# Kernel tuning notes

Hardware: AMD Instinct MI355X
Metric: run time of the kernel (lower is better)

Reference implementation:

```python
import jax, jax.numpy as jnp
import numpy as np

N_NODES = 100000
N_EDGES = 1600000
HIDDEN = 64
N_MID = 3  # num_layers=5 -> 1 first + 3 middle + 1 last


def setup_inputs() -> dict:
    key = jax.random.key(0)
    ks = jax.random.split(key, 12)
    x = jax.random.normal(ks[0], (N_NODES, 1), dtype=jnp.float32)
    edge_index = jax.random.randint(ks[1], (2, N_EDGES), 0, N_NODES, dtype=jnp.int32)
    edge_weight = jax.random.uniform(ks[2], (N_EDGES,), dtype=jnp.float32)
    s0 = 1.0  # fan_in=1
    sh = 1.0 / np.sqrt(HIDDEN)
    Wrel0 = jax.random.normal(ks[3], (HIDDEN, 1), dtype=jnp.float32) * s0
    brel0 = jax.random.normal(ks[4], (HIDDEN,), dtype=jnp.float32) * s0
    Wroot0 = jax.random.normal(ks[5], (HIDDEN, 1), dtype=jnp.float32) * s0
    Wrel_mid = jax.random.normal(ks[6], (N_MID, HIDDEN, HIDDEN), dtype=jnp.float32) * sh
    brel_mid = jax.random.normal(ks[7], (N_MID, HIDDEN), dtype=jnp.float32) * sh
    Wroot_mid = jax.random.normal(ks[8], (N_MID, HIDDEN, HIDDEN), dtype=jnp.float32) * sh
    WrelL = jax.random.normal(ks[9], (1, HIDDEN), dtype=jnp.float32) * sh
    brelL = jax.random.normal(ks[10], (1,), dtype=jnp.float32) * sh
    WrootL = jax.random.normal(ks[11], (1, HIDDEN), dtype=jnp.float32) * sh
    return {"x": x, "edge_index": edge_index, "edge_weight": edge_weight,
            "Wrel0": Wrel0, "brel0": brel0, "Wroot0": Wroot0,
            "Wrel_mid": Wrel_mid, "brel_mid": brel_mid, "Wroot_mid": Wroot_mid,
            "WrelL": WrelL, "brelL": brelL, "WrootL": WrootL}


def reference(x, edge_index, edge_weight, Wrel0, brel0, Wroot0,
              Wrel_mid, brel_mid, Wroot_mid, WrelL, brelL, WrootL):
    src = edge_index[0]
    dst = edge_index[1]
    n = x.shape[0]

    def conv(h, Wrel, brel, Wroot):
        # PyG GraphConv(aggr='add'): lin_rel(sum_j w_ij * h_j) + lin_root(h_i)
        msg = h[src] * edge_weight[:, None]          # [E, C]
        agg = jax.ops.segment_sum(msg, dst, num_segments=n)  # [N, C]
        return agg @ Wrel.T + brel + h @ Wroot.T

    # dropout omitted (deterministic reference); relu after all but last layer
    h = jax.nn.relu(conv(x, Wrel0, brel0, Wroot0))
    for i in range(Wrel_mid.shape[0]):
        h = jax.nn.relu(conv(h, Wrel_mid[i], brel_mid[i], Wroot_mid[i]))
    return conv(h, WrelL, brelL, WrootL)  # [N, 1]
```

## Files before the change

### kernel.cpp

```cpp
#include <hip/hip_runtime.h>
#include <stdint.h>


#define NN 100000
#define NE 1600000
#define HID 64
#define NBKT 391
#define CAP 8192
#define PMAX (NBKT * CAP)
#define TILE 4096
#define EPT 16
#define NTILE ((NE + TILE - 1) / TILE)

typedef __attribute__((ext_vector_type(8))) short bf16x8;
typedef __attribute__((ext_vector_type(4))) float f32x4;
typedef __attribute__((ext_vector_type(2))) unsigned int u32x2;
typedef __attribute__((ext_vector_type(4))) unsigned int u32x4;

__device__ __forceinline__ uint32_t rne_bf16(float v) {
    uint32_t u = __float_as_uint(v);
    return (u + 0x7fffu + ((u >> 16) & 1u)) >> 16;
}


__global__ __launch_bounds__(256) void k_bpart(const int* __restrict__ src,
                                               const int* __restrict__ dst,
                                               const float* __restrict__ w,
                                               int* __restrict__ bcur,
                                               int2* __restrict__ bpairs) {
    __shared__ int  hcnt[NBKT];
    __shared__ int  hoff[NBKT];
    __shared__ int  hadj[NBKT];
    __shared__ int  sc0[512];
    __shared__ int  sc1[512];
    __shared__ int2 sT[TILE];
    __shared__ int  sAdj[TILE];
    int tile0 = blockIdx.x * TILE;
    int t = threadIdx.x;
    for (int i = t; i < NBKT; i += 256) hcnt[i] = 0;
    __syncthreads();

    int   pk[EPT];
    int   bk[EPT];
    float wv[EPT];
    #pragma unroll
    for (int k = 0; k < EPT; k++) {
        int e = tile0 + t + k * 256;
        if (e < NE) {
            int d = dst[e];
            int b = d >> 8;
            pk[k] = (src[e] << 8) | (d & 255);
            wv[k] = w[e];
            bk[k] = b;
            atomicAdd(&hcnt[b], 1);
        } else {
            bk[k] = -1;
        }
    }
    __syncthreads();

    sc0[t]       = (t < NBKT) ? hcnt[t] : 0;
    sc0[t + 256] = (t + 256 < NBKT) ? hcnt[t + 256] : 0;
    __syncthreads();
    int* cur = sc0;
    int* oth = sc1;
    for (int off = 1; off < 512; off <<= 1) {
        int v0 = cur[t]       + ((t       >= off) ? cur[t - off]       : 0);
        int v1 = cur[t + 256] + ((t + 256 >= off) ? cur[t + 256 - off] : 0);
        oth[t] = v0;
        oth[t + 256] = v1;
        __syncthreads();
        int* tmp = cur; cur = oth; oth = tmp;
    }
    for (int i = t; i < NBKT; i += 256) {
        int c = hcnt[i];
        int excl = cur[i] - c;
        hoff[i] = excl;
        int gbase = c ? atomicAdd(&bcur[i], c) : 0;
        hadj[i] = gbase - excl;
        hcnt[i] = 0;
    }
    __syncthreads();

    #pragma unroll
    for (int k = 0; k < EPT; k++) {
        if (bk[k] >= 0) {
            int b = bk[k];
            int pos = hoff[b] + atomicAdd(&hcnt[b], 1);
            sT[pos] = make_int2(pk[k], __float_as_int(wv[k]));
            sAdj[pos] = hadj[b];
        }
    }
    __syncthreads();

    int n = NE - tile0; if (n > TILE) n = TILE;
    for (int j = t; j < n; j += 256)
        bpairs[sAdj[j] + j] = sT[j];
}

__global__ __launch_bounds__(256) void k_bcsr(const int* __restrict__ bcur,
                                              const int2* __restrict__ bpairs,
                                              int* __restrict__ offs,
                                              int* __restrict__ ends,
                                              uint32_t* __restrict__ pairs) {
    __shared__ int2 sE[CAP];
    __shared__ int cnt[256];
    __shared__ int scn[256];
    __shared__ int cur[256];
    int k = blockIdx.x, t = threadIdx.x;
    int base = k * CAP;
    int scnt = bcur[k] - base;
    cnt[t] = 0;
    __syncthreads();
    for (int j = t; j < scnt; j += 256) {
        int2 q = bpairs[base + j];
        sE[j] = q;
        atomicAdd(&cnt[q.x & 255], 1);
    }
    __syncthreads();
    int v = cnt[t], acc = v;
    scn[t] = v;
    __syncthreads();
    for (int off = 1; off < 256; off <<= 1) {
        int u = (t >= off) ? scn[t - off] : 0;
        __syncthreads();
        acc += u;
        scn[t] = acc;
        __syncthreads();
    }
    int excl = acc - v;
    cur[t] = excl;
    int d = (k << 8) + t;
    if (d < NN) {
        offs[d] = base + excl;
        ends[d] = base + excl + v;
    }
    __syncthreads();
    for (int j = t; j < scnt; j += 256) {
        int2 q = sE[j];
        int pos = base + atomicAdd(&cur[q.x & 255], 1);
        uint32_t wb = rne_bf16(__int_as_float(q.y)) & 0x7fffu;
        pairs[pos] = (wb << 17) | (uint32_t)(q.x >> 8);
    }
}


__global__ __launch_bounds__(256) void k_wsplit(const float* __restrict__ Wrel_mid,
                                                const float* __restrict__ Wroot_mid,
                                                uint16_t* __restrict__ WgH,
                                                uint16_t* __restrict__ WgL,
                                                uint16_t* __restrict__ WrH,
                                                uint16_t* __restrict__ WrL,
                                                int* __restrict__ bcur) {
    int i = blockIdx.x * blockDim.x + threadIdx.x;
    if (i < NBKT) bcur[i] = i * CAP;
    if (i >= 3 * 4096) return;
    float a = Wrel_mid[i];
    uint32_t ah = rne_bf16(a);
    float al = a - __uint_as_float(ah << 16);
    WgH[i] = (uint16_t)ah;
    WgL[i] = (uint16_t)rne_bf16(al);
    float b = Wroot_mid[i];
    uint32_t bh = rne_bf16(b);
    float bl = b - __uint_as_float(bh << 16);
    WrH[i] = (uint16_t)bh;
    WrL[i] = (uint16_t)rne_bf16(bl);
}


__device__ __forceinline__ void mfma_epilogue(
        int lane, int w, const uint32_t* sH,
        const uint16_t* __restrict__ WgH, const uint16_t* __restrict__ WgL,
        const uint16_t* __restrict__ WrH, const uint16_t* __restrict__ WrL,
        const float* __restrict__ brel,
        uint16_t* sG, uint16_t* sR) {
    int row = lane & 15;
    int quad = lane >> 4;
    int kb = quad * 8;
    bf16x8 ah0 = *(const bf16x8*)&sH[row * 36 + quad * 4];
    bf16x8 ah1 = *(const bf16x8*)&sH[row * 36 + 16 + quad * 4];
    int oc = w * 16 + row;
    {
        bf16x8 bh0 = *(const bf16x8*)&WgH[oc * 64 + kb];
        bf16x8 bh1 = *(const bf16x8*)&WgH[oc * 64 + 32 + kb];
        bf16x8 bl0 = *(const bf16x8*)&WgL[oc * 64 + kb];
        bf16x8 bl1 = *(const bf16x8*)&WgL[oc * 64 + 32 + kb];
        f32x4 acc = {0.f, 0.f, 0.f, 0.f};
        acc = __builtin_amdgcn_mfma_f32_16x16x32_bf16(ah0, bh0, acc, 0, 0, 0);
        acc = __builtin_amdgcn_mfma_f32_16x16x32_bf16(ah1, bh1, acc, 0, 0, 0);
        acc = __builtin_amdgcn_mfma_f32_16x16x32_bf16(ah0, bl0, acc, 0, 0, 0);
        acc = __builtin_amdgcn_mfma_f32_16x16x32_bf16(ah1, bl1, acc, 0, 0, 0);
        #pragma unroll
        for (int r = 0; r < 4; r++)
            sG[(quad * 4 + r) * 68 + oc] = (uint16_t)rne_bf16(acc[r]);
    }
    {
        bf16x8 bh0 = *(const bf16x8*)&WrH[oc * 64 + kb];
        bf16x8 bh1 = *(const bf16x8*)&WrH[oc * 64 + 32 + kb];
        bf16x8 bl0 = *(const bf16x8*)&WrL[oc * 64 + kb];
        bf16x8 bl1 = *(const bf16x8*)&WrL[oc * 64 + 32 + kb];
        float bias = brel[oc];
        f32x4 acc = {bias, bias, bias, bias};
        acc = __builtin_amdgcn_mfma_f32_16x16x32_bf16(ah0, bh0, acc, 0, 0, 0);
        acc = __builtin_amdgcn_mfma_f32_16x16x32_bf16(ah1, bh1, acc, 0, 0, 0);
        acc = __builtin_amdgcn_mfma_f32_16x16x32_bf16(ah0, bl0, acc, 0, 0, 0);
        acc = __builtin_amdgcn_mfma_f32_16x16x32_bf16(ah1, bl1, acc, 0, 0, 0);
        #pragma unroll
        for (int r = 0; r < 4; r++)
            sR[(quad * 4 + r) * 68 + oc] = (uint16_t)rne_bf16(acc[r]);
    }
}

__device__ __forceinline__ void epilogue_writeout(
        int tid, int blk16, const uint16_t* sG, const uint16_t* sR,
        uint16_t* __restrict__ Gout, uint16_t* __restrict__ Rout) {
    const uint32_t* sGd = (const uint32_t*)sG;
    const uint32_t* sRd = (const uint32_t*)sR;
    uint32_t* Gd = (uint32_t*)Gout;
    uint32_t* Rd = (uint32_t*)Rout;
    #pragma unroll
    for (int it = 0; it < 2; it++) {
        int idx = it * 256 + tid;
        int nd = idx >> 5, col = idx & 31;
        Gd[(blk16 + nd) * 32 + col] = sGd[nd * 34 + col];
        Rd[(blk16 + nd) * 32 + col] = sRd[nd * 34 + col];
    }
}


__global__ __launch_bounds__(256) void k_l0pre(
        const int* __restrict__ offs, const int* __restrict__ ends,
        const uint32_t* __restrict__ pairs, const float* __restrict__ x,
        const float* __restrict__ Wrel0, const float* __restrict__ brel0,
        const float* __restrict__ Wroot0,
        const uint16_t* __restrict__ WgH, const uint16_t* __restrict__ WgL,
        const uint16_t* __restrict__ WrH, const uint16_t* __restrict__ WrL,
        const float* __restrict__ brel,
        uint16_t* __restrict__ Gout, uint16_t* __restrict__ Rout) {
    __shared__ uint32_t sH[16 * 36];
    __shared__ uint16_t sG[16 * 68];
    __shared__ uint16_t sR[16 * 68];
    int c = threadIdx.x & 63;
    int w = threadIdx.x >> 6;
    int blk16 = blockIdx.x * 16;
    float agg[4];
    #pragma unroll
    for (int t = 0; t < 4; t++) {
        int node = blk16 + w * 4 + t;
        int b = offs[node], e = ends[node];
        float pp = 0.f;
        for (int j = b + c; j < e; j += 64) {
            uint32_t r = pairs[j];
            pp += __uint_as_float((r >> 17) << 16) * x[r & 0x1ffffu];
        }
        for (int o = 32; o > 0; o >>= 1) pp += __shfl_down(pp, o, 64);
        agg[t] = __shfl(pp, 0, 64);
    }
    float wr = Wrel0[c], br = brel0[c], wo = Wroot0[c];
    #pragma unroll
    for (int t = 0; t < 4; t++) {
        int node = blk16 + w * 4 + t;
        float v = agg[t] * wr + br + x[node] * wo;
        v = v > 0.f ? v : 0.f;
        uint32_t hb = rne_bf16(v);
        uint32_t pn = (uint32_t)__shfl_xor((int)hb, 1, 64);
        if (!(c & 1)) sH[(w * 4 + t) * 36 + (c >> 1)] = hb | (pn << 16);
    }
    __syncthreads();
    mfma_epilogue(c, w, sH, WgH, WgL, WrH, WrL, brel, sG, sR);
    __syncthreads();
    epilogue_writeout((int)threadIdx.x, blk16, sG, sR, Gout, Rout);
}

#define TRRA(dst, off) \
    asm volatile("ds_read_b64_tr_b16 %0, %1 offset:" #off \
                 : "=v"(dst) : "v"(trbA))
#define TRRB(dst, off) \
    asm volatile("ds_read_b64_tr_b16 %0, %1 offset:" #off \
                 : "=v"(dst) : "v"(trbB))

template <bool LAST>
__global__ __launch_bounds__(64, 5) void k_aggfused(
        const int* __restrict__ offs, const int* __restrict__ ends,
        const uint32_t* __restrict__ pairs,
        const uint16_t* __restrict__ Gb, const uint16_t* __restrict__ Rb,
        const uint16_t* __restrict__ WgH, const uint16_t* __restrict__ WgL,
        const uint16_t* __restrict__ WrH, const uint16_t* __restrict__ WrL,
        const float* __restrict__ brel,
        uint16_t* __restrict__ Gout, uint16_t* __restrict__ Rout,
        const float* __restrict__ WrelL, const float* __restrict__ WrootL,
        float* __restrict__ sarr, float* __restrict__ rarr) {
    __shared__ __align__(128) char smem[8192];
    int c = threadIdx.x;
    int n0 = blockIdx.x * 16;

    int myNode = n0 + (c & 15);
    int nodeOK = myNode < NN;
    int nclamp = nodeOK ? myNode : NN - 1;
    int blo = offs[nclamp];
    int bhi = nodeOK ? ends[nclamp] : blo;
    uint32_t wid = (uint32_t)(bhi - blo);
    int start  = __builtin_amdgcn_readlane(blo, 0);
    int finish = __builtin_amdgcn_readlane(bhi, 15);

    int kq = (c >> 4) * 8;
    int eprm  = ((c >> 5) << 2) | ((c >> 1) & 3);
    int lbyte = ((c >> 3) & 3) * 32 + (c & 1) * 16;
    char* stg = smem;
    uint32_t stgOff = (uint32_t)(uintptr_t)
        (__attribute__((address_space(3))) char*)stg;
    uint32_t trbA = stgOff + ((uint32_t)(c >> 4) << 10)
                          + ((uint32_t)(c & 15) << 3);
    uint32_t trbB = trbA + 4096;

    f32x4 acc16[4];
    #pragma unroll
    for (int nb = 0; nb < 4; nb++) {
        #pragma unroll
        for (int t = 0; t < 4; t++) {
            int node = n0 + (c >> 4) * 4 + t;
            int ncl = node < NN ? node : NN - 1;
            uint32_t rv = (uint32_t)Rb[ncl * 64 + nb * 16 + (c & 15)];
            acc16[nb][t] = __uint_as_float(rv << 16);
        }
    }

    const char* gbase = (const char*)Gb;
    int j0 = start + c; if (j0 > PMAX - 1) j0 = PMAX - 1;
    uint32_t praw = pairs[j0];
    uint32_t p = (start + c < finish) ? praw : 0;

    for (int cb = start; cb < finish; cb += 64) {
        int jn = cb + 64 + c; if (jn > PMAX - 1) jn = PMAX - 1;
        uint32_t pr2 = pairs[jn];
        #pragma unroll
        for (int i = 0; i < 4; i++) {
            uint32_t r = (uint32_t)__builtin_amdgcn_ds_bpermute(
                (eprm + i * 8) * 4, (int)p);
            uint32_t voff = ((r & 0x1ffffu) << 7) + (uint32_t)lbyte;
            __builtin_amdgcn_global_load_lds(
                (const __attribute__((address_space(1))) void*)(gbase + voff),
                (__attribute__((address_space(3))) void*)(stg + i * 1024),
                16, 0, 0);
        }
        #pragma unroll
        for (int i = 0; i < 4; i++) {
            uint32_t r = (uint32_t)__builtin_amdgcn_ds_bpermute(
                (32 + eprm + i * 8) * 4, (int)p);
            uint32_t voff = ((r & 0x1ffffu) << 7) + (uint32_t)lbyte;
            __builtin_amdgcn_global_load_lds(
                (const __attribute__((address_space(1))) void*)(gbase + voff),
                (__attribute__((address_space(3))) void*)(stg + 4096 + i * 1024),
                16, 0, 0);
        }
        uint32_t mA[8], mB[8];
        int dbA = cb + kq - blo;
        int dbB = cb + 32 + kq - blo;
        #pragma unroll
        for (int q = 0; q < 8; q++) {
            uint32_t rq = (uint32_t)__builtin_amdgcn_ds_bpermute(
                (kq + q) * 4, (int)p);
            mA[q] = ((uint32_t)(dbA + q) < wid) ? (rq >> 17) : 0u;
        }
        #pragma unroll
        for (int q = 0; q < 8; q++) {
            uint32_t rq = (uint32_t)__builtin_amdgcn_ds_bpermute(
                (32 + kq + q) * 4, (int)p);
            mB[q] = ((uint32_t)(dbB + q) < wid) ? (rq >> 17) : 0u;
        }
        u32x4 aav = { mA[0] | (mA[1] << 16), mA[2] | (mA[3] << 16),
                      mA[4] | (mA[5] << 16), mA[6] | (mA[7] << 16) };
        u32x4 abv = { mB[0] | (mB[1] << 16), mB[2] | (mB[3] << 16),
                      mB[4] | (mB[5] << 16), mB[6] | (mB[7] << 16) };
        bf16x8 afA = __builtin_bit_cast(bf16x8, aav);
        bf16x8 afB = __builtin_bit_cast(bf16x8, abv);
        asm volatile("s_waitcnt vmcnt(4)" ::: "memory");
        {
            u32x2 tb0, tb1, tb2, tb3, tb4, tb5, tb6, tb7;
            TRRA(tb0, 0);   TRRA(tb1, 512);
            TRRA(tb2, 128); TRRA(tb3, 640);
            TRRA(tb4, 256); TRRA(tb5, 768);
            TRRA(tb6, 384); TRRA(tb7, 896);
            asm volatile("s_waitcnt lgkmcnt(0)" ::: "memory");
            __builtin_amdgcn_sched_barrier(0);
            u32x4 bb0 = { tb0.x, tb0.y, tb1.x, tb1.y };
            acc16[0] = __builtin_amdgcn_mfma_f32_16x16x32_bf16(
                afA, __builtin_bit_cast(bf16x8, bb0), acc16[0], 0, 0, 0);
            u32x4 bb1 = { tb2.x, tb2.y, tb3.x, tb3.y };
            acc16[1] = __builtin_amdgcn_mfma_f32_16x16x32_bf16(
                afA, __builtin_bit_cast(bf16x8, bb1), acc16[1], 0, 0, 0);
            u32x4 bb2 = { tb4.x, tb4.y, tb5.x, tb5.y };
            acc16[2] = __builtin_amdgcn_mfma_f32_16x16x32_bf16(
                afA, __builtin_bit_cast(bf16x8, bb2), acc16[2], 0, 0, 0);
            u32x4 bb3 = { tb6.x, tb6.y, tb7.x, tb7.y };
            acc16[3] = __builtin_amdgcn_mfma_f32_16x16x32_bf16(
                afA, __builtin_bit_cast(bf16x8, bb3), acc16[3], 0, 0, 0);
        }
        asm volatile("s_waitcnt vmcnt(0)" ::: "memory");
        {
            u32x2 tb0, tb1, tb2, tb3, tb4, tb5, tb6, tb7;
            TRRB(tb0, 0);   TRRB(tb1, 512);
            TRRB(tb2, 128); TRRB(tb3, 640);
            TRRB(tb4, 256); TRRB(tb5, 768);
            TRRB(tb6, 384); TRRB(tb7, 896);
            asm volatile("s_waitcnt lgkmcnt(0)" ::: "memory");
            __builtin_amdgcn_sched_barrier(0);
            u32x4 bb0 = { tb0.x, tb0.y, tb1.x, tb1.y };
            acc16[0] = __builtin_amdgcn_mfma_f32_16x16x32_bf16(
                afB, __builtin_bit_cast(bf16x8, bb0), acc16[0], 0, 0, 0);
            u32x4 bb1 = { tb2.x, tb2.y, tb3.x, tb3.y };
            acc16[1] = __builtin_amdgcn_mfma_f32_16x16x32_bf16(
                afB, __builtin_bit_cast(bf16x8, bb1), acc16[1], 0, 0, 0);
            u32x4 bb2 = { tb4.x, tb4.y, tb5.x, tb5.y };
            acc16[2] = __builtin_amdgcn_mfma_f32_16x16x32_bf16(
                afB, __builtin_bit_cast(bf16x8, bb2), acc16[2], 0, 0, 0);
            u32x4 bb3 = { tb6.x, tb6.y, tb7.x, tb7.y };
            acc16[3] = __builtin_amdgcn_mfma_f32_16x16x32_bf16(
                afB, __builtin_bit_cast(bf16x8, bb3), acc16[3], 0, 0, 0);
        }
        p = (cb + 64 + c < finish) ? pr2 : 0;
    }

    if (!LAST) {
        uint32_t* sHw = (uint32_t*)smem;
        #pragma unroll
        for (int t = 0; t < 4; t++) {
            #pragma unroll
            for (int nb = 0; nb < 4; nb++) {
                float v = acc16[nb][t];
                v = v > 0.f ? v : 0.f;
                uint32_t hb = rne_bf16(v);
                uint32_t pn2 = (uint32_t)__shfl_xor((int)hb, 1, 64);
                if (!(c & 1))
                    sHw[((c >> 4) * 4 + t) * 36 + nb * 8 + ((c & 15) >> 1)]
                        = hb | (pn2 << 16);
            }
        }
        asm volatile("s_waitcnt lgkmcnt(0)" ::: "memory");
        __builtin_amdgcn_sched_barrier(0);
        uint16_t* sGw = (uint16_t*)(smem + 2304);
        uint16_t* sRw = (uint16_t*)(smem + 2304 + 2176);
        int row = c & 15;
        int quad = c >> 4;
        int kb = quad * 8;
        bf16x8 ah0 = *(const bf16x8*)&sHw[row * 36 + quad * 4];
        bf16x8 ah1 = *(const bf16x8*)&sHw[row * 36 + 16 + quad * 4];
        #pragma unroll
        for (int ob = 0; ob < 4; ob++) {
            int oc = ob * 16 + row;
            {
                bf16x8 bh0 = *(const bf16x8*)&WgH[oc * 64 + kb];
                bf16x8 bh1 = *(const bf16x8*)&WgH[oc * 64 + 32 + kb];
                bf16x8 bl0 = *(const bf16x8*)&WgL[oc * 64 + kb];
                bf16x8 bl1 = *(const bf16x8*)&WgL[oc * 64 + 32 + kb];
                f32x4 acc = {0.f, 0.f, 0.f, 0.f};
                acc = __builtin_amdgcn_mfma_f32_16x16x32_bf16(ah0, bh0, acc, 0, 0, 0);
                acc = __builtin_amdgcn_mfma_f32_16x16x32_bf16(ah1, bh1, acc, 0, 0, 0);
                acc = __builtin_amdgcn_mfma_f32_16x16x32_bf16(ah0, bl0, acc, 0, 0, 0);
                acc = __builtin_amdgcn_mfma_f32_16x16x32_bf16(ah1, bl1, acc, 0, 0, 0);
                #pragma unroll
                for (int r = 0; r < 4; r++)
                    sGw[(quad * 4 + r) * 68 + oc] = (uint16_t)rne_bf16(acc[r]);
            }
            {
                bf16x8 bh0 = *(const bf16x8*)&WrH[oc * 64 + kb];
                bf16x8 bh1 = *(const bf16x8*)&WrH[oc * 64 + 32 + kb];
                bf16x8 bl0 = *(const bf16x8*)&WrL[oc * 64 + kb];
                bf16x8 bl1 = *(const bf16x8*)&WrL[oc * 64 + 32 + kb];
                float bias = brel[oc];
                f32x4 acc = {bias, bias, bias, bias};
                acc = __builtin_amdgcn_mfma_f32_16x16x32_bf16(ah0, bh0, acc, 0, 0, 0);
                acc = __builtin_amdgcn_mfma_f32_16x16x32_bf16(ah1, bh1, acc, 0, 0, 0);
                acc = __builtin_amdgcn_mfma_f32_16x16x32_bf16(ah0, bl0, acc, 0, 0, 0);
                acc = __builtin_amdgcn_mfma_f32_16x16x32_bf16(ah1, bl1, acc, 0, 0, 0);
                #pragma unroll
                for (int r = 0; r < 4; r++)
                    sRw[(quad * 4 + r) * 68 + oc] = (uint16_t)rne_bf16(acc[r]);
            }
        }
        asm volatile("s_waitcnt lgkmcnt(0)" ::: "memory");
        __builtin_amdgcn_sched_barrier(0);
        const uint32_t* sGd = (const uint32_t*)sGw;
        const uint32_t* sRd = (const uint32_t*)sRw;
        uint32_t* Gd = (uint32_t*)Gout;
        uint32_t* Rd = (uint32_t*)Rout;
        #pragma unroll
        for (int it = 0; it < 8; it++) {
            int idx = it * 64 + c;
            int nd = idx >> 5, col = idx & 31;
            int node = n0 + nd;
            if (node < NN) {
                Gd[node * 32 + col] = sGd[nd * 34 + col];
                Rd[node * 32 + col] = sRd[nd * 34 + col];
            }
        }
    } else {
        float wl[4], wo[4];
        #pragma unroll
        for (int nb = 0; nb < 4; nb++) {
            wl[nb] = WrelL[nb * 16 + (c & 15)];
            wo[nb] = WrootL[nb * 16 + (c & 15)];
        }
        #pragma unroll
        for (int t = 0; t < 4; t++) {
            float pa = 0.f, pr = 0.f;
            #pragma unroll
            for (int nb = 0; nb < 4; nb++) {
                float v = acc16[nb][t];
                v = v > 0.f ? v : 0.f;
                pa += v * wl[nb];
                pr += v * wo[nb];
            }
            #pragma unroll
            for (int o = 8; o > 0; o >>= 1) {
                pa += __shfl_down(pa, o, 64);
                pr += __shfl_down(pr, o, 64);
            }
            int node = n0 + (c >> 4) * 4 + t;
            if (!(c & 15) && node < NN) { sarr[node] = pa; rarr[node] = pr; }
        }
    }
}

__global__ __launch_bounds__(256) void k_last(
        const int* __restrict__ offs, const int* __restrict__ ends,
        const uint32_t* __restrict__ pairs,
        const float* __restrict__ sarr, const float* __restrict__ rarr,
        const float* __restrict__ brelL, float* __restrict__ out) {
    int c = threadIdx.x & 63;
    int w = threadIdx.x >> 6;
    int blk16 = blockIdx.x * 16;
    float b0 = brelL[0];
    #pragma unroll
    for (int t = 0; t < 4; t++) {
        int node = blk16 + w * 4 + t;
        int b = offs[node], e = ends[node];
        float pp = 0.f;
        for (int j = b + c; j < e; j += 64) {
            uint32_t r = pairs[j];
            pp += __uint_as_float((r >> 17) << 16) * sarr[r & 0x1ffffu];
        }
        #pragma unroll
        for (int o = 32; o > 0; o >>= 1) pp += __shfl_down(pp, o, 64);
        if (c == 0) out[node] = pp + rarr[node] + b0;
    }
}

extern "C" void kernel_launch(void* const* d_in, const int* in_sizes, int n_in,
                              void* d_out, int out_size, void* d_ws, size_t ws_size,
                              hipStream_t stream) {
    const float* x        = (const float*)d_in[0];
    const int*   ei       = (const int*)d_in[1];
    const float* ew       = (const float*)d_in[2];
    const float* Wrel0    = (const float*)d_in[3];
    const float* brel0    = (const float*)d_in[4];
    const float* Wroot0   = (const float*)d_in[5];
    const float* Wrel_mid = (const float*)d_in[6];
    const float* brel_mid = (const float*)d_in[7];
    const float* Wroot_mid= (const float*)d_in[8];
    const float* WrelL    = (const float*)d_in[9];
    const float* brelL    = (const float*)d_in[10];
    const float* WrootL   = (const float*)d_in[11];
    float* out = (float*)d_out;

    const int* src  = ei;
    const int* dstp = ei + NE;

    char* w = (char*)d_ws;
    size_t o = 0;
    auto alloc = [&](size_t b) -> void* {
        void* r = (void*)(w + o);
        o += (b + 255) & ~(size_t)255;
        return r;
    };
    int*      offs  = (int*)alloc((size_t)NN * 4);
    int*      ends  = (int*)alloc((size_t)NN * 4);
    int*      bcur  = (int*)alloc((size_t)NBKT * 4);
    uint16_t* WgH   = (uint16_t*)alloc((size_t)3 * 4096 * 2);
    uint16_t* WgL   = (uint16_t*)alloc((size_t)3 * 4096 * 2);
    uint16_t* WrH   = (uint16_t*)alloc((size_t)3 * 4096 * 2);
    uint16_t* WrL   = (uint16_t*)alloc((size_t)3 * 4096 * 2);
    float*    sarr  = (float*)alloc((size_t)NN * 4);
    float*    rarr  = (float*)alloc((size_t)NN * 4);
    uint32_t* pairs = (uint32_t*)alloc((size_t)NBKT * CAP * 4);
    uint16_t* GbA   = (uint16_t*)alloc((size_t)NN * HID * 2);
    uint16_t* RbA   = (uint16_t*)alloc((size_t)NN * HID * 2);
    uint16_t* GbB   = (uint16_t*)alloc((size_t)NN * HID * 2);
    uint16_t* RbB   = (uint16_t*)alloc((size_t)NN * HID * 2);
    (void)RbB;
    int2*  bpairs = (int2*)GbB;

    k_wsplit<<<(3 * 4096 + 255) / 256, 256, 0, stream>>>(
        Wrel_mid, Wroot_mid, WgH, WgL, WrH, WrL, bcur);

    k_bpart<<<NTILE, 256, 0, stream>>>(src, dstp, ew, bcur, bpairs);
    k_bcsr<<<NBKT, 256, 0, stream>>>(bcur, bpairs, offs, ends, pairs);

    k_l0pre<<<NN / 16, 256, 0, stream>>>(
        offs, ends, pairs, x, Wrel0, brel0, Wroot0,
        WgH, WgL, WrH, WrL, brel_mid, GbA, RbA);

    int nagg = (NN + 15) / 16;
    k_aggfused<false><<<nagg, 64, 0, stream>>>(
        offs, ends, pairs, GbA, RbA,
        WgH + 4096, WgL + 4096, WrH + 4096, WrL + 4096, brel_mid + HID,
        GbB, RbB, WrelL, WrootL, sarr, rarr);
    k_aggfused<false><<<nagg, 64, 0, stream>>>(
        offs, ends, pairs, GbB, RbB,
        WgH + 2 * 4096, WgL + 2 * 4096, WrH + 2 * 4096, WrL + 2 * 4096,
        brel_mid + 2 * HID, GbA, RbA, WrelL, WrootL, sarr, rarr);
    k_aggfused<true><<<nagg, 64, 0, stream>>>(
        offs, ends, pairs, GbA, RbA,
        WgH, WgL, WrH, WrL, brel_mid,
        GbB, RbB, WrelL, WrootL, sarr, rarr);

    k_last<<<NN / 16, 256, 0, stream>>>(offs, ends, pairs, sarr, rarr, brelL, out);
}
```

Measured before the change: 297.6 us.

## Double-buffer gathered neighbor rows in LDS to overlap loads with MFMA

Gives the fused aggregation kernel's gather staging two LDS buffers (16 KB instead of 8 KB). It issues the global_load_lds gathers for the next 64-edge chunk before consuming the current chunk with MFMAs, and prefetches edge pairs two chunks ahead. The aim is to hide gather latency behind compute instead of waiting on vmcnt within each chunk. In exchange, the launch-bounds occupancy hint drops from 5 to 4 blocks and LDS use per block doubles, which may reduce the waves available to hide latency.

```diff
diff --git a/kernel.cpp b/kernel.cpp
--- a/kernel.cpp
+++ b/kernel.cpp
@@ -272,15 +272,12 @@
     epilogue_writeout((int)threadIdx.x, blk16, sG, sR, Gout, Rout);
 }
 
-#define TRRA(dst, off) \
+#define TRR(dst, base, off) \
     asm volatile("ds_read_b64_tr_b16 %0, %1 offset:" #off \
-                 : "=v"(dst) : "v"(trbA))
-#define TRRB(dst, off) \
-    asm volatile("ds_read_b64_tr_b16 %0, %1 offset:" #off \
-                 : "=v"(dst) : "v"(trbB))
+                 : "=v"(dst) : "v"(base))
 
 template <bool LAST>
-__global__ __launch_bounds__(64, 5) void k_aggfused(
+__global__ __launch_bounds__(64, 4) void k_aggfused(
         const int* __restrict__ offs, const int* __restrict__ ends,
         const uint32_t* __restrict__ pairs,
         const uint16_t* __restrict__ Gb, const uint16_t* __restrict__ Rb,
@@ -290,7 +287,7 @@
         uint16_t* __restrict__ Gout, uint16_t* __restrict__ Rout,
         const float* __restrict__ WrelL, const float* __restrict__ WrootL,
         float* __restrict__ sarr, float* __restrict__ rarr) {
-    __shared__ __align__(128) char smem[8192];
+    __shared__ __align__(128) char smem[16384];
     int c = threadIdx.x;
     int n0 = blockIdx.x * 16;
 
@@ -306,12 +303,10 @@
     int kq = (c >> 4) * 8;
     int eprm  = ((c >> 5) << 2) | ((c >> 1) & 3);
     int lbyte = ((c >> 3) & 3) * 32 + (c & 1) * 16;
-    char* stg = smem;
     uint32_t stgOff = (uint32_t)(uintptr_t)
-        (__attribute__((address_space(3))) char*)stg;
-    uint32_t trbA = stgOff + ((uint32_t)(c >> 4) << 10)
+        (__attribute__((address_space(3))) char*)smem;
+    uint32_t trb0 = stgOff + ((uint32_t)(c >> 4) << 10)
                           + ((uint32_t)(c & 15) << 3);
-    uint32_t trbB = trbA + 4096;
 
     f32x4 acc16[4];
     #pragma unroll
@@ -326,100 +321,124 @@
     }
 
     const char* gbase = (const char*)Gb;
-    int j0 = start + c; if (j0 > PMAX - 1) j0 = PMAX - 1;
-    uint32_t praw = pairs[j0];
-    uint32_t p = (start + c < finish) ? praw : 0;
-
-    for (int cb = start; cb < finish; cb += 64) {
-        int jn = cb + 64 + c; if (jn > PMAX - 1) jn = PMAX - 1;
-        uint32_t pr2 = pairs[jn];
+
+    auto ISSUE8 = [&](uint32_t pp, int s) {
+        char* dst = smem + (s ? 8192 : 0);
         #pragma unroll
         for (int i = 0; i < 4; i++) {
             uint32_t r = (uint32_t)__builtin_amdgcn_ds_bpermute(
-                (eprm + i * 8) * 4, (int)p);
+                (eprm + i * 8) * 4, (int)pp);
             uint32_t voff = ((r & 0x1ffffu) << 7) + (uint32_t)lbyte;
             __builtin_amdgcn_global_load_lds(
                 (const __attribute__((address_space(1))) void*)(gbase + voff),
-                (__attribute__((address_space(3))) void*)(stg + i * 1024),
+                (__attribute__((address_space(3))) void*)(dst + i * 1024),
                 16, 0, 0);
         }
         #pragma unroll
         for (int i = 0; i < 4; i++) {
             uint32_t r = (uint32_t)__builtin_amdgcn_ds_bpermute(
-                (32 + eprm + i * 8) * 4, (int)p);
+                (32 + eprm + i * 8) * 4, (int)pp);
             uint32_t voff = ((r & 0x1ffffu) << 7) + (uint32_t)lbyte;
             __builtin_amdgcn_global_load_lds(
                 (const __attribute__((address_space(1))) void*)(gbase + voff),
-                (__attribute__((address_space(3))) void*)(stg + 4096 + i * 1024),
+                (__attribute__((address_space(3))) void*)(dst + 4096 + i * 1024),
                 16, 0, 0);
         }
+    };
+
+    auto CONSUME = [&](int s, bf16x8 afA, bf16x8 afB) {
+        uint32_t ta = trb0 + (s ? 8192u : 0u);
+        uint32_t tb = ta + 4096u;
+        u32x2 a0, a1, a2, a3, a4, a5, a6, a7;
+        TRR(a0, ta, 0);   TRR(a1, ta, 512);
+        TRR(a2, ta, 128); TRR(a3, ta, 640);
+        TRR(a4, ta, 256); TRR(a5, ta, 768);
+        TRR(a6, ta, 384); TRR(a7, ta, 896);
+        u32x2 b0, b1, b2, b3, b4, b5, b6, b7;
+        TRR(b0, tb, 0);   TRR(b1, tb, 512);
+        TRR(b2, tb, 128); TRR(b3, tb, 640);
+        TRR(b4, tb, 256); TRR(b5, tb, 768);
+        TRR(b6, tb, 384); TRR(b7, tb, 896);
+        asm volatile("s_waitcnt lgkmcnt(0)" ::: "memory");
+        __builtin_amdgcn_sched_barrier(0);
+        u32x4 v0 = { a0.x, a0.y, a1.x, a1.y };
+        acc16[0] = __builtin_amdgcn_mfma_f32_16x16x32_bf16(
+            afA, __builtin_bit_cast(bf16x8, v0), acc16[0], 0, 0, 0);
+        u32x4 v1 = { a2.x, a2.y, a3.x, a3.y };
+        acc16[1] = __builtin_amdgcn_mfma_f32_16x16x32_bf16(
+            afA, __builtin_bit_cast(bf16x8, v1), acc16[1], 0, 0, 0);
+        u32x4 v2 = { a4.x, a4.y, a5.x, a5.y };
+        acc16[2] = __builtin_amdgcn_mfma_f32_16x16x32_bf16(
+            afA, __builtin_bit_cast(bf16x8, v2), acc16[2], 0, 0, 0);
+        u32x4 v3 = { a6.x, a6.y, a7.x, a7.y };
+        acc16[3] = __builtin_amdgcn_mfma_f32_16x16x32_bf16(
+            afA, __builtin_bit_cast(bf16x8, v3), acc16[3], 0, 0, 0);
+        u32x4 w0 = { b0.x, b0.y, b1.x, b1.y };
+        acc16[0] = __builtin_amdgcn_mfma_f32_16x16x32_bf16(
+            afB, __builtin_bit_cast(bf16x8, w0), acc16[0], 0, 0, 0);
+        u32x4 w1 = { b2.x, b2.y, b3.x, b3.y };
+        acc16[1] = __builtin_amdgcn_mfma_f32_16x16x32_bf16(
+            afB, __builtin_bit_cast(bf16x8, w1), acc16[1], 0, 0, 0);
+        u32x4 w2 = { b4.x, b4.y, b5.x, b5.y };
+        acc16[2] = __builtin_amdgcn_mfma_f32_16x16x32_bf16(
+            afB, __builtin_bit_cast(bf16x8, w2), acc16[2], 0, 0, 0);
+        u32x4 w3 = { b6.x, b6.y, b7.x, b7.y };
+        acc16[3] = __builtin_amdgcn_mfma_f32_16x16x32_bf16(
+            afB, __builtin_bit_cast(bf16x8, w3), acc16[3], 0, 0, 0);
+    };
+
+    auto AFRAGS = [&](uint32_t pp, int cb, bf16x8& afA, bf16x8& afB) {
         uint32_t mA[8], mB[8];
         int dbA = cb + kq - blo;
         int dbB = cb + 32 + kq - blo;
         #pragma unroll
         for (int q = 0; q < 8; q++) {
             uint32_t rq = (uint32_t)__builtin_amdgcn_ds_bpermute(
-                (kq + q) * 4, (int)p);
+                (kq + q) * 4, (int)pp);
             mA[q] = ((uint32_t)(dbA + q) < wid) ? (rq >> 17) : 0u;
         }
         #pragma unroll
         for (int q = 0; q < 8; q++) {
             uint32_t rq = (uint32_t)__builtin_amdgcn_ds_bpermute(
-                (32 + kq + q) * 4, (int)p);
+                (32 + kq + q) * 4, (int)pp);
             mB[q] = ((uint32_t)(dbB + q) < wid) ? (rq >> 17) : 0u;
         }
         u32x4 aav = { mA[0] | (mA[1] << 16), mA[2] | (mA[3] << 16),
                       mA[4] | (mA[5] << 16), mA[6] | (mA[7] << 16) };
         u32x4 abv = { mB[0] | (mB[1] << 16), mB[2] | (mB[3] << 16),
                       mB[4] | (mB[5] << 16), mB[6] | (mB[7] << 16) };
-        bf16x8 afA = __builtin_bit_cast(bf16x8, aav);
-        bf16x8 afB = __builtin_bit_cast(bf16x8, abv);
-        asm volatile("s_waitcnt vmcnt(4)" ::: "memory");
-        {
-            u32x2 tb0, tb1, tb2, tb3, tb4, tb5, tb6, tb7;
-            TRRA(tb0, 0);   TRRA(tb1, 512);
-            TRRA(tb2, 128); TRRA(tb3, 640);
-            TRRA(tb4, 256); TRRA(tb5, 768);
-            TRRA(tb6, 384); TRRA(tb7, 896);
-            asm volatile("s_waitcnt lgkmcnt(0)" ::: "memory");
-            __builtin_amdgcn_sched_barrier(0);
-            u32x4 bb0 = { tb0.x, tb0.y, tb1.x, tb1.y };
-            acc16[0] = __builtin_amdgcn_mfma_f32_16x16x32_bf16(
-                afA, __builtin_bit_cast(bf16x8, bb0), acc16[0], 0, 0, 0);
-            u32x4 bb1 = { tb2.x, tb2.y, tb3.x, tb3.y };
-            acc16[1] = __builtin_amdgcn_mfma_f32_16x16x32_bf16(
-                afA, __builtin_bit_cast(bf16x8, bb1), acc16[1], 0, 0, 0);
-            u32x4 bb2 = { tb4.x, tb4.y, tb5.x, tb5.y };
-            acc16[2] = __builtin_amdgcn_mfma_f32_16x16x32_bf16(
-                afA, __builtin_bit_cast(bf16x8, bb2), acc16[2], 0, 0, 0);
-            u32x4 bb3 = { tb6.x, tb6.y, tb7.x, tb7.y };
-            acc16[3] = __builtin_amdgcn_mfma_f32_16x16x32_bf16(
-                afA, __builtin_bit_cast(bf16x8, bb3), acc16[3], 0, 0, 0);
-        }
-        asm volatile("s_waitcnt vmcnt(0)" ::: "memory");
-        {
-            u32x2 tb0, tb1, tb2, tb3, tb4, tb5, tb6, tb7;
-            TRRB(tb0, 0);   TRRB(tb1, 512);
-            TRRB(tb2, 128); TRRB(tb3, 640);
-            TRRB(tb4, 256); TRRB(tb5, 768);
-            TRRB(tb6, 384); TRRB(tb7, 896);
-            asm volatile("s_waitcnt lgkmcnt(0)" ::: "memory");
-            __builtin_amdgcn_sched_barrier(0);
-            u32x4 bb0 = { tb0.x, tb0.y, tb1.x, tb1.y };
-            acc16[0] = __builtin_amdgcn_mfma_f32_16x16x32_bf16(
-                afB, __builtin_bit_cast(bf16x8, bb0), acc16[0], 0, 0, 0);
-            u32x4 bb1 = { tb2.x, tb2.y, tb3.x, tb3.y };
-            acc16[1] = __builtin_amdgcn_mfma_f32_16x16x32_bf16(
-                afB, __builtin_bit_cast(bf16x8, bb1), acc16[1], 0, 0, 0);
-            u32x4 bb2 = { tb4.x, tb4.y, tb5.x, tb5.y };
-            acc16[2] = __builtin_amdgcn_mfma_f32_16x16x32_bf16(
-                afB, __builtin_bit_cast(bf16x8, bb2), acc16[2], 0, 0, 0);
-            u32x4 bb3 = { tb6.x, tb6.y, tb7.x, tb7.y };
-            acc16[3] = __builtin_amdgcn_mfma_f32_16x16x32_bf16(
-                afB, __builtin_bit_cast(bf16x8, bb3), acc16[3], 0, 0, 0);
-        }
-        p = (cb + 64 + c < finish) ? pr2 : 0;
-    }
+        afA = __builtin_bit_cast(bf16x8, aav);
+        afB = __builtin_bit_cast(bf16x8, abv);
+    };
+
+    int j0 = start + c; if (j0 > PMAX - 1) j0 = PMAX - 1;
+    uint32_t praw = pairs[j0];
+    asm volatile("s_waitcnt vmcnt(0)" ::: "memory");
+    uint32_t p = (start + c < finish) ? praw : 0;
+    int j1 = start + 64 + c; if (j1 > PMAX - 1) j1 = PMAX - 1;
+    uint32_t pnext = pairs[j1];
+    ISSUE8(p, 0);
+    int sel = 0;
+
+    for (int cb = start; cb < finish; cb += 64) {
+        bf16x8 afA, afB;
+        uint32_t pn = 0, pnext2 = 0;
+        if (cb + 64 < finish) {
+            asm volatile("s_waitcnt vmcnt(8)" ::: "memory");
+            pn = (cb + 64 + c < finish) ? pnext : 0;
+            int j2 = cb + 128 + c; if (j2 > PMAX - 1) j2 = PMAX - 1;
+            pnext2 = pairs[j2];
+            ISSUE8(pn, sel ^ 1);
+            AFRAGS(p, cb, afA, afB);
+            asm volatile("s_waitcnt vmcnt(9)" ::: "memory");
+        } else {
+            AFRAGS(p, cb, afA, afB);
+            asm volatile("s_waitcnt vmcnt(0)" ::: "memory");
+        }
+        CONSUME(sel, afA, afB);
+        p = pn; pnext = pnext2; sel ^= 1;
+    }
+    asm volatile("s_waitcnt vmcnt(0)" ::: "memory");
 
     if (!LAST) {
         uint32_t* sHw = (uint32_t*)smem;
```

After: 317.4 us. 6.7% more time.

## Aggregate raw hidden features instead of pre-transformed G/R projections

Applied to the files above, without the earlier changes.

Previously each layer's epilogue precomputed G = H·Wrel and R = H·Wroot+b per node, and the next layer gathered G along edges. Now only the bf16 hidden state H is written, and the edge aggregation gathers H directly. Each fused kernel then applies both Wrel (to the aggregate) and Wroot (to the node's own H) with MFMA plus ReLU. This halves per-layer output writes and removes the separate R read and buffer, and layer 0 no longer runs MFMAs. The cost is that the aggregate is now rounded to bf16 before the matmul, which changes numerical accuracy, and boundary guards for NN are dropped.

```diff
diff --git a/kernel.cpp b/kernel.cpp
--- a/kernel.cpp
+++ b/kernel.cpp
@@ -168,78 +168,12 @@
 }
 
 
-__device__ __forceinline__ void mfma_epilogue(
-        int lane, int w, const uint32_t* sH,
-        const uint16_t* __restrict__ WgH, const uint16_t* __restrict__ WgL,
-        const uint16_t* __restrict__ WrH, const uint16_t* __restrict__ WrL,
-        const float* __restrict__ brel,
-        uint16_t* sG, uint16_t* sR) {
-    int row = lane & 15;
-    int quad = lane >> 4;
-    int kb = quad * 8;
-    bf16x8 ah0 = *(const bf16x8*)&sH[row * 36 + quad * 4];
-    bf16x8 ah1 = *(const bf16x8*)&sH[row * 36 + 16 + quad * 4];
-    int oc = w * 16 + row;
-    {
-        bf16x8 bh0 = *(const bf16x8*)&WgH[oc * 64 + kb];
-        bf16x8 bh1 = *(const bf16x8*)&WgH[oc * 64 + 32 + kb];
-        bf16x8 bl0 = *(const bf16x8*)&WgL[oc * 64 + kb];
-        bf16x8 bl1 = *(const bf16x8*)&WgL[oc * 64 + 32 + kb];
-        f32x4 acc = {0.f, 0.f, 0.f, 0.f};
-        acc = __builtin_amdgcn_mfma_f32_16x16x32_bf16(ah0, bh0, acc, 0, 0, 0);
-        acc = __builtin_amdgcn_mfma_f32_16x16x32_bf16(ah1, bh1, acc, 0, 0, 0);
-        acc = __builtin_amdgcn_mfma_f32_16x16x32_bf16(ah0, bl0, acc, 0, 0, 0);
-        acc = __builtin_amdgcn_mfma_f32_16x16x32_bf16(ah1, bl1, acc, 0, 0, 0);
-        #pragma unroll
-        for (int r = 0; r < 4; r++)
-            sG[(quad * 4 + r) * 68 + oc] = (uint16_t)rne_bf16(acc[r]);
-    }
-    {
-        bf16x8 bh0 = *(const bf16x8*)&WrH[oc * 64 + kb];
-        bf16x8 bh1 = *(const bf16x8*)&WrH[oc * 64 + 32 + kb];
-        bf16x8 bl0 = *(const bf16x8*)&WrL[oc * 64 + kb];
-        bf16x8 bl1 = *(const bf16x8*)&WrL[oc * 64 + 32 + kb];
-        float bias = brel[oc];
-        f32x4 acc = {bias, bias, bias, bias};
-        acc = __builtin_amdgcn_mfma_f32_16x16x32_bf16(ah0, bh0, acc, 0, 0, 0);
-        acc = __builtin_amdgcn_mfma_f32_16x16x32_bf16(ah1, bh1, acc, 0, 0, 0);
-        acc = __builtin_amdgcn_mfma_f32_16x16x32_bf16(ah0, bl0, acc, 0, 0, 0);
-        acc = __builtin_amdgcn_mfma_f32_16x16x32_bf16(ah1, bl1, acc, 0, 0, 0);
-        #pragma unroll
-        for (int r = 0; r < 4; r++)
-            sR[(quad * 4 + r) * 68 + oc] = (uint16_t)rne_bf16(acc[r]);
-    }
-}
-
-__device__ __forceinline__ void epilogue_writeout(
-        int tid, int blk16, const uint16_t* sG, const uint16_t* sR,
-        uint16_t* __restrict__ Gout, uint16_t* __restrict__ Rout) {
-    const uint32_t* sGd = (const uint32_t*)sG;
-    const uint32_t* sRd = (const uint32_t*)sR;
-    uint32_t* Gd = (uint32_t*)Gout;
-    uint32_t* Rd = (uint32_t*)Rout;
-    #pragma unroll
-    for (int it = 0; it < 2; it++) {
-        int idx = it * 256 + tid;
-        int nd = idx >> 5, col = idx & 31;
-        Gd[(blk16 + nd) * 32 + col] = sGd[nd * 34 + col];
-        Rd[(blk16 + nd) * 32 + col] = sRd[nd * 34 + col];
-    }
-}
-
-
 __global__ __launch_bounds__(256) void k_l0pre(
         const int* __restrict__ offs, const int* __restrict__ ends,
         const uint32_t* __restrict__ pairs, const float* __restrict__ x,
         const float* __restrict__ Wrel0, const float* __restrict__ brel0,
         const float* __restrict__ Wroot0,
-        const uint16_t* __restrict__ WgH, const uint16_t* __restrict__ WgL,
-        const uint16_t* __restrict__ WrH, const uint16_t* __restrict__ WrL,
-        const float* __restrict__ brel,
-        uint16_t* __restrict__ Gout, uint16_t* __restrict__ Rout) {
-    __shared__ uint32_t sH[16 * 36];
-    __shared__ uint16_t sG[16 * 68];
-    __shared__ uint16_t sR[16 * 68];
+        uint16_t* __restrict__ Hout) {
     int c = threadIdx.x & 63;
     int w = threadIdx.x >> 6;
     int blk16 = blockIdx.x * 16;
@@ -257,6 +191,7 @@
         agg[t] = __shfl(pp, 0, 64);
     }
     float wr = Wrel0[c], br = brel0[c], wo = Wroot0[c];
+    uint32_t* Hd = (uint32_t*)Hout;
     #pragma unroll
     for (int t = 0; t < 4; t++) {
         int node = blk16 + w * 4 + t;
@@ -264,12 +199,8 @@
         v = v > 0.f ? v : 0.f;
         uint32_t hb = rne_bf16(v);
         uint32_t pn = (uint32_t)__shfl_xor((int)hb, 1, 64);
-        if (!(c & 1)) sH[(w * 4 + t) * 36 + (c >> 1)] = hb | (pn << 16);
-    }
-    __syncthreads();
-    mfma_epilogue(c, w, sH, WgH, WgL, WrH, WrL, brel, sG, sR);
-    __syncthreads();
-    epilogue_writeout((int)threadIdx.x, blk16, sG, sR, Gout, Rout);
+        if (!(c & 1)) Hd[node * 32 + (c >> 1)] = hb | (pn << 16);
+    }
 }
 
 #define TRRA(dst, off) \
@@ -283,11 +214,11 @@
 __global__ __launch_bounds__(64, 5) void k_aggfused(
         const int* __restrict__ offs, const int* __restrict__ ends,
         const uint32_t* __restrict__ pairs,
-        const uint16_t* __restrict__ Gb, const uint16_t* __restrict__ Rb,
+        const uint16_t* __restrict__ Hb,
         const uint16_t* __restrict__ WgH, const uint16_t* __restrict__ WgL,
         const uint16_t* __restrict__ WrH, const uint16_t* __restrict__ WrL,
         const float* __restrict__ brel,
-        uint16_t* __restrict__ Gout, uint16_t* __restrict__ Rout,
+        uint16_t* __restrict__ Hout,
         const float* __restrict__ WrelL, const float* __restrict__ WrootL,
         float* __restrict__ sarr, float* __restrict__ rarr) {
     __shared__ __align__(128) char smem[8192];
@@ -295,10 +226,8 @@
     int n0 = blockIdx.x * 16;
 
     int myNode = n0 + (c & 15);
-    int nodeOK = myNode < NN;
-    int nclamp = nodeOK ? myNode : NN - 1;
-    int blo = offs[nclamp];
-    int bhi = nodeOK ? ends[nclamp] : blo;
+    int blo = offs[myNode];
+    int bhi = ends[myNode];
     uint32_t wid = (uint32_t)(bhi - blo);
     int start  = __builtin_amdgcn_readlane(blo, 0);
     int finish = __builtin_amdgcn_readlane(bhi, 15);
@@ -315,17 +244,9 @@
 
     f32x4 acc16[4];
     #pragma unroll
-    for (int nb = 0; nb < 4; nb++) {
-        #pragma unroll
-        for (int t = 0; t < 4; t++) {
-            int node = n0 + (c >> 4) * 4 + t;
-            int ncl = node < NN ? node : NN - 1;
-            uint32_t rv = (uint32_t)Rb[ncl * 64 + nb * 16 + (c & 15)];
-            acc16[nb][t] = __uint_as_float(rv << 16);
-        }
-    }
-
-    const char* gbase = (const char*)Gb;
+    for (int nb = 0; nb < 4; nb++) acc16[nb] = f32x4{0.f, 0.f, 0.f, 0.f};
+
+    const char* gbase = (const char*)Hb;
     int j0 = start + c; if (j0 > PMAX - 1) j0 = PMAX - 1;
     uint32_t praw = pairs[j0];
     uint32_t p = (start + c < finish) ? praw : 0;
@@ -420,104 +341,113 @@
         }
         p = (cb + 64 + c < finish) ? pr2 : 0;
     }
+    asm volatile("s_waitcnt vmcnt(0)" ::: "memory");
+
+    int row = c & 15;
+    int quad = c >> 4;
+    int kb = quad * 8;
+    bf16x8 hs0 = *(const bf16x8*)&Hb[(n0 + row) * 64 + kb];
+    bf16x8 hs1 = *(const bf16x8*)&Hb[(n0 + row) * 64 + 32 + kb];
+    uint32_t* sHw = (uint32_t*)smem;
+    #pragma unroll
+    for (int t = 0; t < 4; t++) {
+        #pragma unroll
+        for (int nb = 0; nb < 4; nb++) {
+            uint32_t hb = rne_bf16(acc16[nb][t]);
+            uint32_t pn2 = (uint32_t)__shfl_xor((int)hb, 1, 64);
+            if (!(c & 1))
+                sHw[(quad * 4 + t) * 36 + nb * 8 + (row >> 1)]
+                    = hb | (pn2 << 16);
+        }
+    }
+    asm volatile("s_waitcnt lgkmcnt(0)" ::: "memory");
+    __builtin_amdgcn_sched_barrier(0);
+    bf16x8 ah0 = *(const bf16x8*)&sHw[row * 36 + quad * 4];
+    bf16x8 ah1 = *(const bf16x8*)&sHw[row * 36 + 16 + quad * 4];
 
     if (!LAST) {
-        uint32_t* sHw = (uint32_t*)smem;
-        #pragma unroll
-        for (int t = 0; t < 4; t++) {
+        uint16_t* sO = (uint16_t*)(smem + 2304);
+        #pragma unroll
+        for (int ob = 0; ob < 4; ob++) {
+            int oc = ob * 16 + row;
+            float bias = brel[oc];
+            f32x4 acc = {bias, bias, bias, bias};
+            bf16x8 gh0 = *(const bf16x8*)&WgH[oc * 64 + kb];
+            bf16x8 gh1 = *(const bf16x8*)&WgH[oc * 64 + 32 + kb];
+            bf16x8 gl0 = *(const bf16x8*)&WgL[oc * 64 + kb];
+            bf16x8 gl1 = *(const bf16x8*)&WgL[oc * 64 + 32 + kb];
+            acc = __builtin_amdgcn_mfma_f32_16x16x32_bf16(ah0, gh0, acc, 0, 0, 0);
+            acc = __builtin_amdgcn_mfma_f32_16x16x32_bf16(ah1, gh1, acc, 0, 0, 0);
+            acc = __builtin_amdgcn_mfma_f32_16x16x32_bf16(ah0, gl0, acc, 0, 0, 0);
+            acc = __builtin_amdgcn_mfma_f32_16x16x32_bf16(ah1, gl1, acc, 0, 0, 0);
+            bf16x8 rh0 = *(const bf16x8*)&WrH[oc * 64 + kb];
+            bf16x8 rh1 = *(const bf16x8*)&WrH[oc * 64 + 32 + kb];
+            bf16x8 rl0 = *(const bf16x8*)&WrL[oc * 64 + kb];
+            bf16x8 rl1 = *(const bf16x8*)&WrL[oc * 64 + 32 + kb];
+            acc = __builtin_amdgcn_mfma_f32_16x16x32_bf16(hs0, rh0, acc, 0, 0, 0);
+            acc = __builtin_amdgcn_mfma_f32_16x16x32_bf16(hs1, rh1, acc, 0, 0, 0);
+            acc = __builtin_amdgcn_mfma_f32_16x16x32_bf16(hs0, rl0, acc, 0, 0, 0);
+            acc = __builtin_amdgcn_mfma_f32_16x16x32_bf16(hs1, rl1, acc, 0, 0, 0);
             #pragma unroll
-            for (int nb = 0; nb < 4; nb++) {
-                float v = acc16[nb][t];
-                v = v > 0.f ? v : 0.f;
-                uint32_t hb = rne_bf16(v);
-                uint32_t pn2 = (uint32_t)__shfl_xor((int)hb, 1, 64);
-                if (!(c & 1))
-                    sHw[((c >> 4) * 4 + t) * 36 + nb * 8 + ((c & 15) >> 1)]
-                        = hb | (pn2 << 16);
+            for (int r = 0; r < 4; r++) {
+                float v = acc[r] > 0.f ? acc[r] : 0.f;
+                sO[(quad * 4 + r) * 68 + oc] = (uint16_t)rne_bf16(v);
             }
         }
         asm volatile("s_waitcnt lgkmcnt(0)" ::: "memory");
         __builtin_amdgcn_sched_barrier(0);
-        uint16_t* sGw = (uint16_t*)(smem + 2304);
-        uint16_t* sRw = (uint16_t*)(smem + 2304 + 2176);
-        int row = c & 15;
-        int quad = c >> 4;
-        int kb = quad * 8;
-        bf16x8 ah0 = *(const bf16x8*)&sHw[row * 36 + quad * 4];
-        bf16x8 ah1 = *(const bf16x8*)&sHw[row * 36 + 16 + quad * 4];
-        #pragma unroll
-        for (int ob = 0; ob < 4; ob++) {
-            int oc = ob * 16 + row;
-            {
-                bf16x8 bh0 = *(const bf16x8*)&WgH[oc * 64 + kb];
-                bf16x8 bh1 = *(const bf16x8*)&WgH[oc * 64 + 32 + kb];
-                bf16x8 bl0 = *(const bf16x8*)&WgL[oc * 64 + kb];
-                bf16x8 bl1 = *(const bf16x8*)&WgL[oc * 64 + 32 + kb];
-                f32x4 acc = {0.f, 0.f, 0.f, 0.f};
-                acc = __builtin_amdgcn_mfma_f32_16x16x32_bf16(ah0, bh0, acc, 0, 0, 0);
-                acc = __builtin_amdgcn_mfma_f32_16x16x32_bf16(ah1, bh1, acc, 0, 0, 0);
-                acc = __builtin_amdgcn_mfma_f32_16x16x32_bf16(ah0, bl0, acc, 0, 0, 0);
-                acc = __builtin_amdgcn_mfma_f32_16x16x32_bf16(ah1, bl1, acc, 0, 0, 0);
-                #pragma unroll
-                for (int r = 0; r < 4; r++)
-                    sGw[(quad * 4 + r) * 68 + oc] = (uint16_t)rne_bf16(acc[r]);
-            }
-            {
-                bf16x8 bh0 = *(const bf16x8*)&WrH[oc * 64 + kb];
-                bf16x8 bh1 = *(const bf16x8*)&WrH[oc * 64 + 32 + kb];
-                bf16x8 bl0 = *(const bf16x8*)&WrL[oc * 64 + kb];
-                bf16x8 bl1 = *(const bf16x8*)&WrL[oc * 64 + 32 + kb];
-                float bias = brel[oc];
-                f32x4 acc = {bias, bias, bias, bias};
-                acc = __builtin_amdgcn_mfma_f32_16x16x32_bf16(ah0, bh0, acc, 0, 0, 0);
-                acc = __builtin_amdgcn_mfma_f32_16x16x32_bf16(ah1, bh1, acc, 0, 0, 0);
-                acc = __builtin_amdgcn_mfma_f32_16x16x32_bf16(ah0, bl0, acc, 0, 0, 0);
-                acc = __builtin_amdgcn_mfma_f32_16x16x32_bf16(ah1, bl1, acc, 0, 0, 0);
-                #pragma unroll
-                for (int r = 0; r < 4; r++)
-                    sRw[(quad * 4 + r) * 68 + oc] = (uint16_t)rne_bf16(acc[r]);
-            }
-        }
-        asm volatile("s_waitcnt lgkmcnt(0)" ::: "memory");
-        __builtin_amdgcn_sched_barrier(0);
-        const uint32_t* sGd = (const uint32_t*)sGw;
-        const uint32_t* sRd = (const uint32_t*)sRw;
-        uint32_t* Gd = (uint32_t*)Gout;
-        uint32_t* Rd = (uint32_t*)Rout;
+        const uint32_t* sOd = (const uint32_t*)sO;
+        uint32_t* Hd = (uint32_t*)Hout;
         #pragma unroll
         for (int it = 0; it < 8; it++) {
             int idx = it * 64 + c;
             int nd = idx >> 5, col = idx & 31;
-            int node = n0 + nd;
-            if (node < NN) {
-                Gd[node * 32 + col] = sGd[nd * 34 + col];
-                Rd[node * 32 + col] = sRd[nd * 34 + col];
+            Hd[(n0 + nd) * 32 + col] = sOd[nd * 34 + col];
+        }
+    } else {
+        float pa[4] = {0.f, 0.f, 0.f, 0.f};
+        float pr[4] = {0.f, 0.f, 0.f, 0.f};
+        #pragma unroll
+        for (int ob = 0; ob < 4; ob++) {
+            int oc = ob * 16 + row;
+            float bias = brel[oc];
+            f32x4 acc = {bias, bias, bias, bias};
+            bf16x8 gh0 = *(const bf16x8*)&WgH[oc * 64 + kb];
+            bf16x8 gh1 = *(const bf16x8*)&WgH[oc * 64 + 32 + kb];
+            bf16x8 gl0 = *(const bf16x8*)&WgL[oc * 64 + kb];
+            bf16x8 gl1 = *(const bf16x8*)&WgL[oc * 64 + 32 + kb];
+            acc = __builtin_amdgcn_mfma_f32_16x16x32_bf16(ah0, gh0, acc, 0, 0, 0);
+            acc = __builtin_amdgcn_mfma_f32_16x16x32_bf16(ah1, gh1, acc, 0, 0, 0);
+            acc = __builtin_amdgcn_mfma_f32_16x16x32_bf16(ah0, gl0, acc, 0, 0, 0);
+            acc = __builtin_amdgcn_mfma_f32_16x16x32_bf16(ah1, gl1, acc, 0, 0, 0);
+            bf16x8 rh0 = *(const bf16x8*)&WrH[oc * 64 + kb];
+            bf16x8 rh1 = *(const bf16x8*)&WrH[oc * 64 + 32 + kb];
+            bf16x8 rl0 = *(const bf16x8*)&WrL[oc * 64 + kb];
+            bf16x8 rl1 = *(const bf16x8*)&WrL[oc * 64 + 32 + kb];
+            acc = __builtin_amdgcn_mfma_f32_16x16x32_bf16(hs0, rh0, acc, 0, 0, 0);
+            acc = __builtin_amdgcn_mfma_f32_16x16x32_bf16(hs1, rh1, acc, 0, 0, 0);
+            acc = __builtin_amdgcn_mfma_f32_16x16x32_bf16(hs0, rl0, acc, 0, 0, 0);
+            acc = __builtin_amdgcn_mfma_f32_16x16x32_bf16(hs1, rl1, acc, 0, 0, 0);
+            float wlc = WrelL[oc], woc = WrootL[oc];
+            #pragma unroll
+            for (int r = 0; r < 4; r++) {
+                float v = acc[r] > 0.f ? acc[r] : 0.f;
+                pa[r] += v * wlc;
+                pr[r] += v * woc;
             }
         }
-    } else {
-        float wl[4], wo[4];
-        #pragma unroll
-        for (int nb = 0; nb < 4; nb++) {
-            wl[nb] = WrelL[nb * 16 + (c & 15)];
-            wo[nb] = WrootL[nb * 16 + (c & 15)];
-        }
-        #pragma unroll
-        for (int t = 0; t < 4; t++) {
-            float pa = 0.f, pr = 0.f;
-            #pragma unroll
-            for (int nb = 0; nb < 4; nb++) {
-                float v = acc16[nb][t];
-                v = v > 0.f ? v : 0.f;
-                pa += v * wl[nb];
-                pr += v * wo[nb];
-            }
+        #pragma unroll
+        for (int r = 0; r < 4; r++) {
             #pragma unroll
             for (int o = 8; o > 0; o >>= 1) {
-                pa += __shfl_down(pa, o, 64);
-                pr += __shfl_down(pr, o, 64);
+                pa[r] += __shfl_down(pa[r], o, 16);
+                pr[r] += __shfl_down(pr[r], o, 16);
             }
-            int node = n0 + (c >> 4) * 4 + t;
-            if (!(c & 15) && node < NN) { sarr[node] = pa; rarr[node] = pr; }
+            if (row == 0) {
+                int node = n0 + quad * 4 + r;
+                sarr[node] = pa[r];
+                rarr[node] = pr[r];
+            }
         }
     }
 }
@@ -583,12 +513,11 @@
     float*    sarr  = (float*)alloc((size_t)NN * 4);
     float*    rarr  = (float*)alloc((size_t)NN * 4);
     uint32_t* pairs = (uint32_t*)alloc((size_t)NBKT * CAP * 4);
-    uint16_t* GbA   = (uint16_t*)alloc((size_t)NN * HID * 2);
-    uint16_t* RbA   = (uint16_t*)alloc((size_t)NN * HID * 2);
-    uint16_t* GbB   = (uint16_t*)alloc((size_t)NN * HID * 2);
-    uint16_t* RbB   = (uint16_t*)alloc((size_t)NN * HID * 2);
-    (void)RbB;
-    int2*  bpairs = (int2*)GbB;
+    uint16_t* HbA   = (uint16_t*)alloc((size_t)NN * HID * 2);
+    uint16_t* HbB   = (uint16_t*)alloc((size_t)NN * HID * 2);
+    uint16_t* spare = (uint16_t*)alloc((size_t)NN * HID * 2);
+    (void)spare;
+    int2*  bpairs = (int2*)HbB;
 
     k_wsplit<<<(3 * 4096 + 255) / 256, 256, 0, stream>>>(
         Wrel_mid, Wroot_mid, WgH, WgL, WrH, WrL, bcur);
@@ -597,22 +526,22 @@
     k_bcsr<<<NBKT, 256, 0, stream>>>(bcur, bpairs, offs, ends, pairs);
 
     k_l0pre<<<NN / 16, 256, 0, stream>>>(
-        offs, ends, pairs, x, Wrel0, brel0, Wroot0,
-        WgH, WgL, WrH, WrL, brel_mid, GbA, RbA);
-
-    int nagg = (NN + 15) / 16;
+        offs, ends, pairs, x, Wrel0, brel0, Wroot0, HbA);
+
+    int nagg = NN / 16;
     k_aggfused<false><<<nagg, 64, 0, stream>>>(
-        offs, ends, pairs, GbA, RbA,
+        offs, ends, pairs, HbA,
+        WgH, WgL, WrH, WrL, brel_mid,
+        HbB, WrelL, WrootL, sarr, rarr);
+    k_aggfused<false><<<nagg, 64, 0, stream>>>(
+        offs, ends, pairs, HbB,
         WgH + 4096, WgL + 4096, WrH + 4096, WrL + 4096, brel_mid + HID,
-        GbB, RbB, WrelL, WrootL, sarr, rarr);
-    k_aggfused<false><<<nagg, 64, 0, stream>>>(
-        offs, ends, pairs, GbB, RbB,
+        HbA, WrelL, WrootL, sarr, rarr);
+    k_aggfused<true><<<nagg, 64, 0, stream>>>(
+        offs, ends, pairs, HbA,
         WgH + 2 * 4096, WgL + 2 * 4096, WrH + 2 * 4096, WrL + 2 * 4096,
-        brel_mid + 2 * HID, GbA, RbA, WrelL, WrootL, sarr, rarr);
-    k_aggfused<true><<<nagg, 64, 0, stream>>>(
-        offs, ends, pairs, GbA, RbA,
-        WgH, WgL, WrH, WrL, brel_mid,
-        GbB, RbB, WrelL, WrootL, sarr, rarr);
+        brel_mid + 2 * HID,
+        HbB, WrelL, WrootL, sarr, rarr);
 
     k_last<<<NN / 16, 256, 0, stream>>>(offs, ends, pairs, sarr, rarr, brelL, out);
 }
```

After: 288.5 us. 1.03x faster.
